# Kernel optimization log

Measured on AMD Instinct MI355X. Metric: run time of the kernel, lower is better.

Reference implementation:

```python
import jax, jax.numpy as jnp
import numpy as np

BATCH, SEQ, D_MODEL = 4, 8192, 2048
NUM_HEADS, NUM_RATES = 32, 6
HEAD_DIM = D_MODEL // NUM_HEADS


def setup_inputs() -> dict:
    key = jax.random.key(0)
    x = jax.random.normal(key, (BATCH, SEQ, D_MODEL), dtype=jnp.float32)
    return {"x": x}


def reference(x) -> jnp.ndarray:
    B, L, D = x.shape
    H, hd = NUM_HEADS, HEAD_DIM
    scale = 1.0 / jnp.sqrt(jnp.asarray(hd, x.dtype))
    outputs = jnp.zeros((B, L, D), dtype=x.dtype)
    denoms = jnp.zeros((B, L, H), dtype=x.dtype)
    for i in range(NUM_RATES):
        dil = 2 ** i          # dilation rate
        seg = 2 ** i          # segment size
        n = L // dil // seg   # segments per dilation offset
        # gather all dilation offsets at once: (B, dil, L//dil, D)
        xo = x.reshape(B, L // dil, dil, D).transpose(0, 2, 1, 3)
        # split into segments and heads: (B, dil, n, seg, H, hd)
        xs = xo.reshape(B, dil, n, seg, H, hd)
        scores = jnp.einsum('bonqhd,bonkhd->bonhqk', xs * scale, xs)
        probs = jax.nn.softmax(scores, axis=-1)
        out = jnp.einsum('bonhqk,bonkhd->bonqhd', probs, xs)
        # per-query softmax denominator (stable): (B, dil, n, seg, H)
        den = jnp.swapaxes(jnp.exp(jax.nn.logsumexp(scores, axis=-1)), -1, -2)
        # scatter-add back onto the full sequence (inverse of the strided gather)
        out_full = out.reshape(B, dil, L // dil, D).transpose(0, 2, 1, 3).reshape(B, L, D)
        den_full = den.reshape(B, dil, L // dil, H).transpose(0, 2, 1, 3).reshape(B, L, H)
        outputs = outputs + out_full
        denoms = denoms + den_full
    # softmax-weighted combine over heads (per token), broadcast over head_dim
    w = jax.nn.softmax(denoms, axis=-1)  # (B, L, H)
    return (outputs.reshape(B, L, H, hd) * w[..., None]).reshape(B, L, D)
```

## Files before the change

kernel.cpp:

```cpp
#include <hip/hip_runtime.h>

#define B_   4
#define L_   8192
#define D_   2048
#define H_   32
#define WIN_ 1024
#define U_   512
#define PAD_ 68

template <int CTRL>
__device__ __forceinline__ float dpp_add(float v) {
    int s = __builtin_amdgcn_update_dpp(0, __builtin_bit_cast(int, v), CTRL, 0xf, 0xf, true);
    return v + __builtin_bit_cast(float, s);
}
__device__ __forceinline__ float sum16(float v) {
    v = dpp_add<0xB1>(v);
    v = dpp_add<0x4E>(v);
    v = dpp_add<0x141>(v);
    v = dpp_add<0x140>(v);
    return v;
}

__device__ __forceinline__ float dot4(const float4& A, const float4& R) {
    float a = 0.f, b = 0.f;
    a = fmaf(A.x, R.x, a); b = fmaf(A.y, R.y, b);
    a = fmaf(A.z, R.z, a); b = fmaf(A.w, R.w, b);
    return a + b;
}

__device__ __forceinline__ void fma4(float4& a, float s, const float4& b) {
    a.x = fmaf(s, b.x, a.x); a.y = fmaf(s, b.y, a.y);
    a.z = fmaf(s, b.z, a.z); a.w = fmaf(s, b.w, a.w);
}

__global__ __launch_bounds__(1024)
void ddattn_k1(const float* __restrict__ x, float* __restrict__ out,
               float* __restrict__ den) {
    const int bid = blockIdx.x;
    const int h   = bid & 31;
    const int p   = (bid >> 5) & 1;
    const int win = (bid >> 6) & 7;
    const int b   = bid >> 9;

    __shared__ float Xs[U_ * PAD_];
    const int t0 = win * WIN_;
    const float* xb = x + ((size_t)b * L_ + (size_t)(t0 + p)) * D_ + h * 64;

    for (int idx = threadIdx.x; idx < U_ * 16; idx += 1024) {
        const int row = idx >> 4, c = idx & 15;
        *(float4*)(&Xs[row * PAD_ + c * 4]) =
            *(const float4*)(xb + (size_t)row * (2 * D_) + c * 4);
    }
    __syncthreads();

    const int lane16 = threadIdx.x & 15;
    const int j      = threadIdx.x >> 4;
    const int off    = lane16 * 4;

#pragma unroll 1
    for (int qq = 0; qq < 4; qq++) {
        const int P  = qq * 64 + j;
        const int u0 = (P & 15) | ((P >> 4) << 5);
        const int u1 = u0 + 16;

        float4 Q0 = *(const float4*)(&Xs[u0 * PAD_ + off]);
        float4 Q1 = *(const float4*)(&Xs[u1 * PAD_ + off]);

        float4 acc0 = Q0, acc1 = Q1;
        float den0 = __expf(sum16(dot4(Q0, Q0)) * 0.125f);
        float den1 = __expf(sum16(dot4(Q1, Q1)) * 0.125f);

        auto rate_single = [&](const float4& Q, int u, float4& acc, float& dn, int i) {
            const int step = 1 << (i - 1), cnt = 1 << i;
            const int ub = ((u >> (2 * i - 1)) << (2 * i - 1)) | (u & (step - 1));
            float4 E = make_float4(0, 0, 0, 0);
            float Dr = 0.f;
            for (int k = 0; k < cnt; k++) {
                const float4 R = *(const float4*)(&Xs[(ub + k * step) * PAD_ + off]);
                const float e = __expf(sum16(dot4(Q, R)) * 0.125f);
                Dr += e;
                fma4(E, e, R);
            }
            dn += Dr;
            fma4(acc, 1.0f / Dr, E);
        };
        rate_single(Q0, u0, acc0, den0, 1);
        rate_single(Q0, u0, acc0, den0, 2);
        rate_single(Q1, u1, acc1, den1, 1);
        rate_single(Q1, u1, acc1, den1, 2);

#pragma unroll
        for (int i = 3; i <= 5; i++) {
            const int step = 1 << (i - 1), cnt = 1 << i;
            const int ub = ((u0 >> (2 * i - 1)) << (2 * i - 1)) | (u0 & (step - 1));
            float4 E0 = make_float4(0, 0, 0, 0), E1 = make_float4(0, 0, 0, 0);
            float D0 = 0.f, D1 = 0.f;
#pragma unroll 4
            for (int k = 0; k < cnt; k++) {
                const float4 R = *(const float4*)(&Xs[(ub + k * step) * PAD_ + off]);
                const float e0 = __expf(sum16(dot4(Q0, R)) * 0.125f);
                const float e1 = __expf(sum16(dot4(Q1, R)) * 0.125f);
                D0 += e0; D1 += e1;
                fma4(E0, e0, R); fma4(E1, e1, R);
            }
            den0 += D0; den1 += D1;
            fma4(acc0, 1.0f / D0, E0);
            fma4(acc1, 1.0f / D1, E1);
        }

        const int tA = t0 + 2 * u0 + p;
        float* opA = out + ((size_t)b * L_ + tA) * D_ + h * 64 + off;
        *(float4*)opA = acc0;
        if (lane16 == 0) den[((size_t)b * L_ + tA) * H_ + h] = den0;

        const int tB = t0 + 2 * u1 + p;
        float* opB = out + ((size_t)b * L_ + tB) * D_ + h * 64 + off;
        *(float4*)opB = acc1;
        if (lane16 == 0) den[((size_t)b * L_ + tB) * H_ + h] = den1;
    }
}

__global__ __launch_bounds__(256)
void ddattn_k2(float* __restrict__ out, const float* __restrict__ den) {
    const int tok0 = blockIdx.x * 2;
    __shared__ float sden[2][H_];
    __shared__ float w2[2][H_];
    if (threadIdx.x < 64)
        sden[threadIdx.x >> 5][threadIdx.x & 31] = den[(size_t)tok0 * H_ + threadIdx.x];
    __syncthreads();
    if (threadIdx.x < 64) {
        const int tt = threadIdx.x >> 5, hh = threadIdx.x & 31;
        float mx = -3.4e38f;
#pragma unroll
        for (int k = 0; k < H_; k++) mx = fmaxf(mx, sden[tt][k]);
        float s = 0.f;
#pragma unroll
        for (int k = 0; k < H_; k++) s += __expf(sden[tt][k] - mx);
        w2[tt][hh] = __expf(sden[tt][hh] - mx) / s;
    }
    __syncthreads();

    float4* o4 = (float4*)(out + (size_t)tok0 * D_);
#pragma unroll
    for (int c = 0; c < 4; c++) {
        const int idx = threadIdx.x + 256 * c;
        const float w = w2[idx >> 9][(idx >> 4) & 31];
        float4 vv = o4[idx];
        vv.x *= w; vv.y *= w; vv.z *= w; vv.w *= w;
        o4[idx] = vv;
    }
}

extern "C" void kernel_launch(void* const* d_in, const int* in_sizes, int n_in,
                              void* d_out, int out_size, void* d_ws, size_t ws_size,
                              hipStream_t stream) {
    const float* x = (const float*)d_in[0];
    float* out = (float*)d_out;
    float* den = (float*)d_ws;

    ddattn_k1<<<dim3(B_ * (L_ / WIN_) * 2 * H_), dim3(1024), 0, stream>>>(x, out, den);
    ddattn_k2<<<dim3(B_ * L_ / 2), dim3(256), 0, stream>>>(out, den);
}
```

Before: 962.1 us.

## Use 8 lanes per query with 8-wide dot products and bigger k2 blocks

The attention kernel now assigns 8 lanes per query instead of 16, so each lane handles 8 head-dim elements. This cuts the DPP reduction from four steps to three and halves the query iterations per thread. The query is also prescaled once, which removes the multiply by 0.125 on every score. The combine kernel now processes 16 tokens per 1024-thread block instead of 2 tokens per 256-thread block, lowering launch and block overhead. Register pressure per thread rises, which may reduce occupancy.

```diff
diff --git a/kernel.cpp b/kernel.cpp
--- a/kernel.cpp
+++ b/kernel.cpp
@@ -7,30 +7,36 @@
 #define WIN_ 1024
 #define U_   512
 #define PAD_ 68
+#define QSC  0.125f
 
 template <int CTRL>
 __device__ __forceinline__ float dpp_add(float v) {
     int s = __builtin_amdgcn_update_dpp(0, __builtin_bit_cast(int, v), CTRL, 0xf, 0xf, true);
     return v + __builtin_bit_cast(float, s);
 }
-__device__ __forceinline__ float sum16(float v) {
+__device__ __forceinline__ float red8(float v) {
     v = dpp_add<0xB1>(v);
     v = dpp_add<0x4E>(v);
     v = dpp_add<0x141>(v);
-    v = dpp_add<0x140>(v);
     return v;
 }
 
-__device__ __forceinline__ float dot4(const float4& A, const float4& R) {
-    float a = 0.f, b = 0.f;
-    a = fmaf(A.x, R.x, a); b = fmaf(A.y, R.y, b);
-    a = fmaf(A.z, R.z, a); b = fmaf(A.w, R.w, b);
-    return a + b;
+__device__ __forceinline__ float dot8(const float4& a0, const float4& a1,
+                                      const float4& b0, const float4& b1) {
+    float s = a0.x * b0.x, t = a0.y * b0.y;
+    s = fmaf(a0.z, b0.z, s); t = fmaf(a0.w, b0.w, t);
+    s = fmaf(a1.x, b1.x, s); t = fmaf(a1.y, b1.y, t);
+    s = fmaf(a1.z, b1.z, s); t = fmaf(a1.w, b1.w, t);
+    return s + t;
 }
 
 __device__ __forceinline__ void fma4(float4& a, float s, const float4& b) {
     a.x = fmaf(s, b.x, a.x); a.y = fmaf(s, b.y, a.y);
     a.z = fmaf(s, b.z, a.z); a.w = fmaf(s, b.w, a.w);
+}
+
+__device__ __forceinline__ float4 mul4(const float4& a, float s) {
+    return make_float4(a.x * s, a.y * s, a.z * s, a.w * s);
 }
 
 __global__ __launch_bounds__(1024)
@@ -53,98 +59,114 @@
     }
     __syncthreads();
 
-    const int lane16 = threadIdx.x & 15;
-    const int j      = threadIdx.x >> 4;
-    const int off    = lane16 * 4;
+    const int lane8 = threadIdx.x & 7;
+    const int slot  = threadIdx.x >> 3;
+    const int off   = lane8 * 8;
 
 #pragma unroll 1
-    for (int qq = 0; qq < 4; qq++) {
-        const int P  = qq * 64 + j;
+    for (int qq = 0; qq < 2; qq++) {
+        const int P  = qq * 128 + slot;
         const int u0 = (P & 15) | ((P >> 4) << 5);
         const int u1 = u0 + 16;
 
-        float4 Q0 = *(const float4*)(&Xs[u0 * PAD_ + off]);
-        float4 Q1 = *(const float4*)(&Xs[u1 * PAD_ + off]);
+        const float4 Qu00 = *(const float4*)(&Xs[u0 * PAD_ + off]);
+        const float4 Qu01 = *(const float4*)(&Xs[u0 * PAD_ + off + 4]);
+        const float4 Qu10 = *(const float4*)(&Xs[u1 * PAD_ + off]);
+        const float4 Qu11 = *(const float4*)(&Xs[u1 * PAD_ + off + 4]);
 
-        float4 acc0 = Q0, acc1 = Q1;
-        float den0 = __expf(sum16(dot4(Q0, Q0)) * 0.125f);
-        float den1 = __expf(sum16(dot4(Q1, Q1)) * 0.125f);
+        const float4 Qs00 = mul4(Qu00, QSC), Qs01 = mul4(Qu01, QSC);
+        const float4 Qs10 = mul4(Qu10, QSC), Qs11 = mul4(Qu11, QSC);
 
-        auto rate_single = [&](const float4& Q, int u, float4& acc, float& dn, int i) {
+        float4 acc00 = Qu00, acc01 = Qu01, acc10 = Qu10, acc11 = Qu11;
+        float den0 = __expf(red8(dot8(Qs00, Qs01, Qu00, Qu01)));
+        float den1 = __expf(red8(dot8(Qs10, Qs11, Qu10, Qu11)));
+
+        auto rate_single = [&](const float4& qa, const float4& qb, int u,
+                               float4& A0, float4& A1, float& dn, int i) {
             const int step = 1 << (i - 1), cnt = 1 << i;
             const int ub = ((u >> (2 * i - 1)) << (2 * i - 1)) | (u & (step - 1));
-            float4 E = make_float4(0, 0, 0, 0);
+            const float* ptr = &Xs[ub * PAD_ + off];
+            float4 E0 = make_float4(0, 0, 0, 0), E1 = make_float4(0, 0, 0, 0);
             float Dr = 0.f;
             for (int k = 0; k < cnt; k++) {
-                const float4 R = *(const float4*)(&Xs[(ub + k * step) * PAD_ + off]);
-                const float e = __expf(sum16(dot4(Q, R)) * 0.125f);
+                const float4 R0 = *(const float4*)(ptr);
+                const float4 R1 = *(const float4*)(ptr + 4);
+                ptr += step * PAD_;
+                const float e = __expf(red8(dot8(qa, qb, R0, R1)));
                 Dr += e;
-                fma4(E, e, R);
+                fma4(E0, e, R0); fma4(E1, e, R1);
             }
             dn += Dr;
-            fma4(acc, 1.0f / Dr, E);
+            const float inv = 1.0f / Dr;
+            fma4(A0, inv, E0); fma4(A1, inv, E1);
         };
-        rate_single(Q0, u0, acc0, den0, 1);
-        rate_single(Q0, u0, acc0, den0, 2);
-        rate_single(Q1, u1, acc1, den1, 1);
-        rate_single(Q1, u1, acc1, den1, 2);
+        rate_single(Qs00, Qs01, u0, acc00, acc01, den0, 1);
+        rate_single(Qs00, Qs01, u0, acc00, acc01, den0, 2);
+        rate_single(Qs10, Qs11, u1, acc10, acc11, den1, 1);
+        rate_single(Qs10, Qs11, u1, acc10, acc11, den1, 2);
 
 #pragma unroll
         for (int i = 3; i <= 5; i++) {
             const int step = 1 << (i - 1), cnt = 1 << i;
             const int ub = ((u0 >> (2 * i - 1)) << (2 * i - 1)) | (u0 & (step - 1));
-            float4 E0 = make_float4(0, 0, 0, 0), E1 = make_float4(0, 0, 0, 0);
+            const float* ptr = &Xs[ub * PAD_ + off];
+            float4 E00 = make_float4(0, 0, 0, 0), E01 = E00, E10 = E00, E11 = E00;
             float D0 = 0.f, D1 = 0.f;
 #pragma unroll 4
             for (int k = 0; k < cnt; k++) {
-                const float4 R = *(const float4*)(&Xs[(ub + k * step) * PAD_ + off]);
-                const float e0 = __expf(sum16(dot4(Q0, R)) * 0.125f);
-                const float e1 = __expf(sum16(dot4(Q1, R)) * 0.125f);
+                const float4 R0 = *(const float4*)(ptr);
+                const float4 R1 = *(const float4*)(ptr + 4);
+                ptr += step * PAD_;
+                const float e0 = __expf(red8(dot8(Qs00, Qs01, R0, R1)));
+                const float e1 = __expf(red8(dot8(Qs10, Qs11, R0, R1)));
                 D0 += e0; D1 += e1;
-                fma4(E0, e0, R); fma4(E1, e1, R);
+                fma4(E00, e0, R0); fma4(E01, e0, R1);
+                fma4(E10, e1, R0); fma4(E11, e1, R1);
             }
             den0 += D0; den1 += D1;
-            fma4(acc0, 1.0f / D0, E0);
-            fma4(acc1, 1.0f / D1, E1);
+            const float i0 = 1.0f / D0, i1 = 1.0f / D1;
+            fma4(acc00, i0, E00); fma4(acc01, i0, E01);
+            fma4(acc10, i1, E10); fma4(acc11, i1, E11);
         }
 
         const int tA = t0 + 2 * u0 + p;
         float* opA = out + ((size_t)b * L_ + tA) * D_ + h * 64 + off;
-        *(float4*)opA = acc0;
-        if (lane16 == 0) den[((size_t)b * L_ + tA) * H_ + h] = den0;
+        *(float4*)opA = acc00; *(float4*)(opA + 4) = acc01;
+        if (lane8 == 0) den[((size_t)b * L_ + tA) * H_ + h] = den0;
 
         const int tB = t0 + 2 * u1 + p;
         float* opB = out + ((size_t)b * L_ + tB) * D_ + h * 64 + off;
-        *(float4*)opB = acc1;
-        if (lane16 == 0) den[((size_t)b * L_ + tB) * H_ + h] = den1;
+        *(float4*)opB = acc10; *(float4*)(opB + 4) = acc11;
+        if (lane8 == 0) den[((size_t)b * L_ + tB) * H_ + h] = den1;
     }
 }
 
-__global__ __launch_bounds__(256)
+__global__ __launch_bounds__(1024)
 void ddattn_k2(float* __restrict__ out, const float* __restrict__ den) {
-    const int tok0 = blockIdx.x * 2;
-    __shared__ float sden[2][H_];
-    __shared__ float w2[2][H_];
-    if (threadIdx.x < 64)
-        sden[threadIdx.x >> 5][threadIdx.x & 31] = den[(size_t)tok0 * H_ + threadIdx.x];
+    const int tid = threadIdx.x;
+    const size_t t0 = (size_t)blockIdx.x * 16;
+    __shared__ float sden[16][32];
+    __shared__ float sw[16][32];
+    if (tid < 512)
+        (&sden[0][0])[tid] = den[t0 * H_ + tid];
     __syncthreads();
-    if (threadIdx.x < 64) {
-        const int tt = threadIdx.x >> 5, hh = threadIdx.x & 31;
+    if (tid < 512) {
+        const int tt = tid >> 5, hh = tid & 31;
         float mx = -3.4e38f;
 #pragma unroll
         for (int k = 0; k < H_; k++) mx = fmaxf(mx, sden[tt][k]);
         float s = 0.f;
 #pragma unroll
         for (int k = 0; k < H_; k++) s += __expf(sden[tt][k] - mx);
-        w2[tt][hh] = __expf(sden[tt][hh] - mx) / s;
+        sw[tt][hh] = __expf(sden[tt][hh] - mx) / s;
     }
     __syncthreads();
 
-    float4* o4 = (float4*)(out + (size_t)tok0 * D_);
+    float4* o4 = (float4*)(out + t0 * D_);
 #pragma unroll
-    for (int c = 0; c < 4; c++) {
-        const int idx = threadIdx.x + 256 * c;
-        const float w = w2[idx >> 9][(idx >> 4) & 31];
+    for (int c = 0; c < 8; c++) {
+        const int idx = tid + 1024 * c;
+        const float w = sw[idx >> 9][(idx >> 4) & 31];
         float4 vv = o4[idx];
         vv.x *= w; vv.y *= w; vv.z *= w; vv.w *= w;
         o4[idx] = vv;
@@ -159,5 +181,5 @@
     float* den = (float*)d_ws;
 
     ddattn_k1<<<dim3(B_ * (L_ / WIN_) * 2 * H_), dim3(1024), 0, stream>>>(x, out, den);
-    ddattn_k2<<<dim3(B_ * L_ / 2), dim3(256), 0, stream>>>(out, den);
+    ddattn_k2<<<dim3(B_ * L_ / 16), dim3(1024), 0, stream>>>(out, den);
 }
```

New measurement: 1.102 ms. +14.5%, slower.

## Use 8 lanes per query with 8-wide slices instead of paired queries

Applied to the files above, without the earlier changes.

Each query row is now handled by 8 lanes that each own 8 head dimensions, replacing 16 lanes with 4 dims that computed two queries sharing keys. This cuts the cross-lane DPP reduction from four steps to three per score and processes one query per lane group, with the 1/sqrt(d) scale folded into Q up front. The trade-off is that the key-row reuse across two queries is lost and each lane now issues two float4 LDS loads per key.

```diff
diff --git a/kernel.cpp b/kernel.cpp
--- a/kernel.cpp
+++ b/kernel.cpp
@@ -7,30 +7,36 @@
 #define WIN_ 1024
 #define U_   512
 #define PAD_ 68
+#define QSC  0.125f
 
 template <int CTRL>
 __device__ __forceinline__ float dpp_add(float v) {
     int s = __builtin_amdgcn_update_dpp(0, __builtin_bit_cast(int, v), CTRL, 0xf, 0xf, true);
     return v + __builtin_bit_cast(float, s);
 }
-__device__ __forceinline__ float sum16(float v) {
+__device__ __forceinline__ float red8(float v) {
     v = dpp_add<0xB1>(v);
     v = dpp_add<0x4E>(v);
     v = dpp_add<0x141>(v);
-    v = dpp_add<0x140>(v);
     return v;
 }
 
-__device__ __forceinline__ float dot4(const float4& A, const float4& R) {
-    float a = 0.f, b = 0.f;
-    a = fmaf(A.x, R.x, a); b = fmaf(A.y, R.y, b);
-    a = fmaf(A.z, R.z, a); b = fmaf(A.w, R.w, b);
-    return a + b;
+__device__ __forceinline__ float dot8(const float4& a0, const float4& a1,
+                                      const float4& b0, const float4& b1) {
+    float s = a0.x * b0.x, t = a0.y * b0.y;
+    s = fmaf(a0.z, b0.z, s); t = fmaf(a0.w, b0.w, t);
+    s = fmaf(a1.x, b1.x, s); t = fmaf(a1.y, b1.y, t);
+    s = fmaf(a1.z, b1.z, s); t = fmaf(a1.w, b1.w, t);
+    return s + t;
 }
 
 __device__ __forceinline__ void fma4(float4& a, float s, const float4& b) {
     a.x = fmaf(s, b.x, a.x); a.y = fmaf(s, b.y, a.y);
     a.z = fmaf(s, b.z, a.z); a.w = fmaf(s, b.w, a.w);
+}
+
+__device__ __forceinline__ float4 mul4(const float4& a, float s) {
+    return make_float4(a.x * s, a.y * s, a.z * s, a.w * s);
 }
 
 __global__ __launch_bounds__(1024)
@@ -53,70 +59,44 @@
     }
     __syncthreads();
 
-    const int lane16 = threadIdx.x & 15;
-    const int j      = threadIdx.x >> 4;
-    const int off    = lane16 * 4;
+    const int lane8 = threadIdx.x & 7;
+    const int slot  = threadIdx.x >> 3;
+    const int off   = lane8 * 8;
 
 #pragma unroll 1
     for (int qq = 0; qq < 4; qq++) {
-        const int P  = qq * 64 + j;
-        const int u0 = (P & 15) | ((P >> 4) << 5);
-        const int u1 = u0 + 16;
+        const int u = qq * 128 + slot;
 
-        float4 Q0 = *(const float4*)(&Xs[u0 * PAD_ + off]);
-        float4 Q1 = *(const float4*)(&Xs[u1 * PAD_ + off]);
+        float4 acc0 = *(const float4*)(&Xs[u * PAD_ + off]);
+        float4 acc1 = *(const float4*)(&Xs[u * PAD_ + off + 4]);
+        const float4 Qs0 = mul4(acc0, QSC), Qs1 = mul4(acc1, QSC);
+        float dn = __expf(red8(dot8(Qs0, Qs1, acc0, acc1)));
 
-        float4 acc0 = Q0, acc1 = Q1;
-        float den0 = __expf(sum16(dot4(Q0, Q0)) * 0.125f);
-        float den1 = __expf(sum16(dot4(Q1, Q1)) * 0.125f);
-
-        auto rate_single = [&](const float4& Q, int u, float4& acc, float& dn, int i) {
+#pragma unroll
+        for (int i = 1; i <= 5; i++) {
             const int step = 1 << (i - 1), cnt = 1 << i;
             const int ub = ((u >> (2 * i - 1)) << (2 * i - 1)) | (u & (step - 1));
-            float4 E = make_float4(0, 0, 0, 0);
-            float Dr = 0.f;
-            for (int k = 0; k < cnt; k++) {
-                const float4 R = *(const float4*)(&Xs[(ub + k * step) * PAD_ + off]);
-                const float e = __expf(sum16(dot4(Q, R)) * 0.125f);
-                Dr += e;
-                fma4(E, e, R);
-            }
-            dn += Dr;
-            fma4(acc, 1.0f / Dr, E);
-        };
-        rate_single(Q0, u0, acc0, den0, 1);
-        rate_single(Q0, u0, acc0, den0, 2);
-        rate_single(Q1, u1, acc1, den1, 1);
-        rate_single(Q1, u1, acc1, den1, 2);
-
-#pragma unroll
-        for (int i = 3; i <= 5; i++) {
-            const int step = 1 << (i - 1), cnt = 1 << i;
-            const int ub = ((u0 >> (2 * i - 1)) << (2 * i - 1)) | (u0 & (step - 1));
-            float4 E0 = make_float4(0, 0, 0, 0), E1 = make_float4(0, 0, 0, 0);
-            float D0 = 0.f, D1 = 0.f;
+            const float* ptr = &Xs[ub * PAD_ + off];
+            float4 E0 = make_float4(0, 0, 0, 0), E1 = E0;
+            float D = 0.f;
 #pragma unroll 4
             for (int k = 0; k < cnt; k++) {
-                const float4 R = *(const float4*)(&Xs[(ub + k * step) * PAD_ + off]);
-                const float e0 = __expf(sum16(dot4(Q0, R)) * 0.125f);
-                const float e1 = __expf(sum16(dot4(Q1, R)) * 0.125f);
-                D0 += e0; D1 += e1;
-                fma4(E0, e0, R); fma4(E1, e1, R);
+                const float4 R0 = *(const float4*)(ptr);
+                const float4 R1 = *(const float4*)(ptr + 4);
+                ptr += step * PAD_;
+                const float e = __expf(red8(dot8(Qs0, Qs1, R0, R1)));
+                D += e;
+                fma4(E0, e, R0); fma4(E1, e, R1);
             }
-            den0 += D0; den1 += D1;
-            fma4(acc0, 1.0f / D0, E0);
-            fma4(acc1, 1.0f / D1, E1);
+            dn += D;
+            const float inv = 1.0f / D;
+            fma4(acc0, inv, E0); fma4(acc1, inv, E1);
         }
 
-        const int tA = t0 + 2 * u0 + p;
-        float* opA = out + ((size_t)b * L_ + tA) * D_ + h * 64 + off;
-        *(float4*)opA = acc0;
-        if (lane16 == 0) den[((size_t)b * L_ + tA) * H_ + h] = den0;
-
-        const int tB = t0 + 2 * u1 + p;
-        float* opB = out + ((size_t)b * L_ + tB) * D_ + h * 64 + off;
-        *(float4*)opB = acc1;
-        if (lane16 == 0) den[((size_t)b * L_ + tB) * H_ + h] = den1;
+        const int t = t0 + 2 * u + p;
+        float* op = out + ((size_t)b * L_ + t) * D_ + h * 64 + off;
+        *(float4*)op = acc0; *(float4*)(op + 4) = acc1;
+        if (lane8 == 0) den[((size_t)b * L_ + t) * H_ + h] = dn;
     }
 }
 
```

Result: faster. 784.6 us (-18.4%).
